# Optimization experiments

Measured on AMD Instinct MI355X. Metric: run time of the kernel, lower is better.

The kernel has to match this reference:

```python
import jax, jax.numpy as jnp
import numpy as np

B, L, D, H = 2, 2048, 1024, 16
HD = D // H
SCALE = HD ** -0.5


def setup_inputs() -> dict:
    key = jax.random.key(0)
    ks = jax.random.split(key, 11)
    s = D ** -0.5  # torch Linear default init scale (uniform bound)
    return {
        "q": jax.random.normal(ks[0], (B, L, D), jnp.float32),
        "k": jax.random.normal(ks[1], (B, L, D), jnp.float32),
        "v": jax.random.normal(ks[2], (B, L, D), jnp.float32),
        "Wq": jax.random.uniform(ks[3], (D, D), jnp.float32, -s, s),
        "bq": jax.random.uniform(ks[4], (D,), jnp.float32, -s, s),
        "Wk": jax.random.uniform(ks[5], (D, D), jnp.float32, -s, s),
        "bk": jax.random.uniform(ks[6], (D,), jnp.float32, -s, s),
        "Wv": jax.random.uniform(ks[7], (D, D), jnp.float32, -s, s),
        "bv": jax.random.uniform(ks[8], (D,), jnp.float32, -s, s),
        "Wo": jax.random.uniform(ks[9], (D, D), jnp.float32, -s, s),
        "bo": jax.random.uniform(ks[10], (D,), jnp.float32, -s, s),
    }


def reference(q, k, v, Wq, bq, Wk, bk, Wv, bv, Wo, bo):
    b, q_len, _ = q.shape
    # projections; weights stored as (D, D) acting on the right: x @ W + b
    qh = (q @ Wq + bq).reshape(b, q_len, H, HD).transpose(0, 2, 1, 3)  # (B,H,Q,hd)
    kh = (k @ Wk + bk).reshape(b, -1, H, HD).transpose(0, 2, 1, 3)    # (B,H,K,hd)
    vh = (v @ Wv + bv).reshape(b, -1, H, HD).transpose(0, 2, 1, 3)    # (B,H,K,hd)
    att = jnp.einsum("bhqd,bhkd->bhqk", qh * SCALE, kh)               # (B,H,Q,K)
    att = jax.nn.softmax(att, axis=-1)
    out = jnp.einsum("bhqk,bhkd->bhqd", att, vh)                      # (B,H,Q,hd)
    out = out.transpose(0, 2, 1, 3).reshape(b, q_len, D)
    return out @ Wo + bo
```

## Files before the change

### kernel.cpp

```cpp
#include <hip/hip_runtime.h>

namespace {
constexpr int kB  = 2;
constexpr int kL  = 2048;
constexpr int kD  = 1024;
constexpr int kH  = 16;
constexpr int kHD = 64;
constexpr int kM  = kB * kL;
}

typedef _Float16 f16x8 __attribute__((ext_vector_type(8)));
typedef float    f32x16 __attribute__((ext_vector_type(16)));
typedef unsigned int u32;

union Frag16 { uint4 u4; unsigned u[4]; f16x8 v; };

__device__ __forceinline__ unsigned short f2h(float f) {
    return __builtin_bit_cast(unsigned short, (_Float16)f);
}
__device__ __forceinline__ unsigned pk2(float a, float b) {
    return __builtin_bit_cast(unsigned, __builtin_amdgcn_cvt_pkrtz(a, b));
}
__device__ __forceinline__ float max3f(float a, float b, float c) {
    float d;
    asm("v_max3_f32 %0, %1, %2, %3" : "=v"(d) : "v"(a), "v"(b), "v"(c));
    return d;
}

__device__ __forceinline__ void gload16(const void* g, void* l) {
    __builtin_amdgcn_global_load_lds(
        (const __attribute__((address_space(1))) u32*)g,
        (__attribute__((address_space(3))) u32*)(unsigned long long)(__builtin_bit_cast(unsigned long long, l)),
        16, 0, 0);
}

__global__ __launch_bounds__(256) void cast_f16_kernel(
    const float* __restrict__ q, const float* __restrict__ k,
    const float* __restrict__ v, unsigned short* __restrict__ dst)
{
    const float* src = blockIdx.y == 0 ? q : (blockIdx.y == 1 ? k : v);
    unsigned short* d = dst + (size_t)blockIdx.y * ((size_t)kM * kD);
    const size_t i = ((size_t)blockIdx.x * 256 + threadIdx.x) * 8;
    const float4 f0 = *(const float4*)(src + i);
    const float4 f1 = *(const float4*)(src + i + 4);
    _Float16 h[8];
    h[0] = (_Float16)f0.x; h[1] = (_Float16)f0.y;
    h[2] = (_Float16)f0.z; h[3] = (_Float16)f0.w;
    h[4] = (_Float16)f1.x; h[5] = (_Float16)f1.y;
    h[6] = (_Float16)f1.z; h[7] = (_Float16)f1.w;
    *(uint4*)(d + i) = *(uint4*)h;
}

__global__ __launch_bounds__(256) void tcast_kernel(
    const float* __restrict__ W0, const float* __restrict__ W1,
    const float* __restrict__ W2, const float* __restrict__ W3,
    unsigned short* __restrict__ WtBase)
{
    __shared__ _Float16 T[64][68];
    const float* W = blockIdx.z == 0 ? W0 : blockIdx.z == 1 ? W1
                   : blockIdx.z == 2 ? W2 : W3;
    unsigned short* Wt = WtBase + (size_t)blockIdx.z * ((size_t)kD * kD);
    const int k0 = blockIdx.y * 64, n0 = blockIdx.x * 64;
    const int tx = threadIdx.x & 15, ty = threadIdx.x >> 4;
#pragma unroll
    for (int i = 0; i < 4; ++i) {
        const int kk = i * 16 + ty;
        const float4 w = *(const float4*)&W[(size_t)(k0 + kk) * kD + n0 + tx * 4];
        T[tx * 4 + 0][kk] = (_Float16)w.x;
        T[tx * 4 + 1][kk] = (_Float16)w.y;
        T[tx * 4 + 2][kk] = (_Float16)w.z;
        T[tx * 4 + 3][kk] = (_Float16)w.w;
    }
    __syncthreads();
#pragma unroll
    for (int i = 0; i < 4; ++i) {
        const int nn = i * 16 + ty;
        *(ushort4*)&Wt[(size_t)(n0 + nn) * kD + k0 + tx * 4] = *(ushort4*)&T[nn][tx * 4];
    }
}

template <int MODE>
__global__ __launch_bounds__(256) void gemm16_kernel(
    const unsigned short* __restrict__ A, const unsigned short* __restrict__ Wt,
    const float* __restrict__ bias, void* __restrict__ Cv)
{
    __shared__ unsigned short Als[3][128 * 32];
    __shared__ unsigned short Bls[3][128 * 32];

    const int tid = threadIdx.x;
    const int lane = tid & 63;
    const int wid = tid >> 6;
    const int l31 = lane & 31;
    const int hi = lane >> 5;
    const int by = blockIdx.x & 31;
    const int bx = blockIdx.x >> 5;
    const int row0 = by * 128;
    const int col0 = bx * 128;
    const int wr = wid >> 1, wc = wid & 1;

    const int srow = wid * 16 + (lane >> 2);
    const int ssl  = lane & 3;
    const int ssrc = (ssl ^ ((srow >> 1) & 3)) * 8;

    const unsigned short* Abase = A + (size_t)(row0 + srow) * kD + ssrc;
    const unsigned short* Bbase = Wt + (size_t)(col0 + srow) * kD + ssrc;

    f32x16 acc00{}, acc01{}, acc10{}, acc11{};

    auto stage = [&](int kt, int buf) {
        gload16(Abase + kt * 32,                   &Als[buf][(wid * 16) * 32]);
        gload16(Abase + (size_t)64 * kD + kt * 32, &Als[buf][(wid * 16 + 64) * 32]);
        gload16(Bbase + kt * 32,                   &Bls[buf][(wid * 16) * 32]);
        gload16(Bbase + (size_t)64 * kD + kt * 32, &Bls[buf][(wid * 16 + 64) * 32]);
    };

    const int ra0 = wr * 64 + l31;
    const int cb0 = wc * 64 + l31;

    stage(0, 0);
    stage(1, 1);
    int cur = 0, stg = 2;
    for (int kt = 0; kt < 32; ++kt) {
        if (kt < 31) asm volatile("s_waitcnt vmcnt(4)" ::: "memory");
        else         asm volatile("s_waitcnt vmcnt(0)" ::: "memory");
        __builtin_amdgcn_s_barrier();
        if (kt + 2 < 32) {
            stage(kt + 2, stg);
            stg = (stg + 1 == 3) ? 0 : stg + 1;
        }
#pragma unroll
        for (int ks = 0; ks < 2; ++ks) {
            const int slot = (ks << 1) | hi;
            Frag16 a0, a1, b0, b1;
            a0.u4 = *(const uint4*)&Als[cur][ra0 * 32 + ((slot ^ ((ra0 >> 1) & 3)) << 3)];
            a1.u4 = *(const uint4*)&Als[cur][(ra0 + 32) * 32 + ((slot ^ (((ra0 + 32) >> 1) & 3)) << 3)];
            b0.u4 = *(const uint4*)&Bls[cur][cb0 * 32 + ((slot ^ ((cb0 >> 1) & 3)) << 3)];
            b1.u4 = *(const uint4*)&Bls[cur][(cb0 + 32) * 32 + ((slot ^ (((cb0 + 32) >> 1) & 3)) << 3)];
            acc00 = __builtin_amdgcn_mfma_f32_32x32x16_f16(a0.v, b0.v, acc00, 0, 0, 0);
            acc01 = __builtin_amdgcn_mfma_f32_32x32x16_f16(a0.v, b1.v, acc01, 0, 0, 0);
            acc10 = __builtin_amdgcn_mfma_f32_32x32x16_f16(a1.v, b0.v, acc10, 0, 0, 0);
            acc11 = __builtin_amdgcn_mfma_f32_32x32x16_f16(a1.v, b1.v, acc11, 0, 0, 0);
        }
        cur = (cur + 1 == 3) ? 0 : cur + 1;
    }

    const float bias0 = bias[col0 + wc * 64 + l31];
    const float bias1 = bias[col0 + wc * 64 + 32 + l31];

    const f32x16* accs[2][2] = {{&acc00, &acc01}, {&acc10, &acc11}};
#pragma unroll
    for (int rt = 0; rt < 2; ++rt) {
#pragma unroll
        for (int ct = 0; ct < 2; ++ct) {
            const f32x16& acv = *accs[rt][ct];
            const float bb = ct ? bias1 : bias0;
            const int c = col0 + wc * 64 + ct * 32 + l31;
            if (MODE == 2) {
                unsigned short* C = (unsigned short*)Cv;
#pragma unroll
                for (int qd = 0; qd < 4; ++qd) {
                    const int r = row0 + wr * 64 + rt * 32 + 8 * qd + 4 * hi;
                    const int b_ = r >> 11, l_ = r & (kL - 1);
                    ushort4 w;
                    w.x = f2h(acv[4 * qd + 0] + bb);
                    w.y = f2h(acv[4 * qd + 1] + bb);
                    w.z = f2h(acv[4 * qd + 2] + bb);
                    w.w = f2h(acv[4 * qd + 3] + bb);
                    *(ushort4*)&C[((size_t)(b_ * kH + (c >> 6)) * kHD + (c & 63)) * kL + l_] = w;
                }
            } else {
#pragma unroll
                for (int reg = 0; reg < 16; ++reg) {
                    const int r = row0 + wr * 64 + rt * 32 + (reg & 3) + 8 * (reg >> 2) + 4 * hi;
                    const float val = acv[reg] + bb;
                    if (MODE == 0) {
                        ((float*)Cv)[(size_t)r * kD + c] = val;
                    } else {
                        const int b_ = r >> 11, l_ = r & (kL - 1);
                        ((unsigned short*)Cv)[((size_t)(b_ * kH + (c >> 6)) * kL + l_) * kHD + (c & 63)] = f2h(val);
                    }
                }
            }
        }
    }
}

__global__ __launch_bounds__(512) void attn_mfma_kernel(
    const unsigned short* __restrict__ Qh, const unsigned short* __restrict__ Kh,
    const unsigned short* __restrict__ Vt, unsigned short* __restrict__ Opart,
    float2* __restrict__ Stat)
{
    __shared__ unsigned short Kls[4][64 * 64];
    __shared__ unsigned short Vls[4][64 * 64];

    const int lane = threadIdx.x & 63;
    const int wid  = threadIdx.x >> 6;
    const int l31  = lane & 31;
    const int hi   = lane >> 5;

    const int id = blockIdx.x;
    const int j  = id >> 3;
    const int bh = (id & 7) * 4 + (j >> 4);
    const int qt = j & 7;
    const int ks = (j >> 3) & 1;
    const int q = qt * 256 + wid * 32 + l31;

    const size_t qkBase = (size_t)bh * kL * kHD;
    const unsigned short* Qp = Qh + qkBase + (size_t)q * kHD + hi * 8;
    Frag16 qf[4];
#pragma unroll
    for (int d = 0; d < 4; ++d) qf[d].u4 = *(const uint4*)(Qp + d * 16);

    const int srow = wid * 8 + (lane >> 3);
    const int soff = (((lane & 7) ^ (srow & 7)) << 3);
    const unsigned short* Kg = Kh + qkBase + (size_t)srow * kHD + soff;
    const unsigned short* Vg = Vt + (size_t)bh * kHD * kL + (size_t)srow * kL + soff;

    auto stage = [&](int kt, int buf) {
        gload16(Kg + (size_t)(kt * 64) * kHD, &Kls[buf][(wid * 8) * 64]);
        gload16(Vg + kt * 64,                 &Vls[buf][(wid * 8) * 64]);
    };

    auto buildpf = [&](const unsigned* u, Frag16* pf) {
        unsigned t0 = hi ? u[0] : u[2];
        unsigned t1 = hi ? u[1] : u[3];
        unsigned t2 = hi ? u[4] : u[6];
        unsigned t3 = hi ? u[5] : u[7];
        const unsigned r0 = __shfl_xor(t0, 32);
        const unsigned r1 = __shfl_xor(t1, 32);
        const unsigned r2 = __shfl_xor(t2, 32);
        const unsigned r3 = __shfl_xor(t3, 32);
        pf[0].u[0] = hi ? r0 : u[0];
        pf[0].u[1] = hi ? r1 : u[1];
        pf[0].u[2] = hi ? u[2] : r0;
        pf[0].u[3] = hi ? u[3] : r1;
        pf[1].u[0] = hi ? r2 : u[4];
        pf[1].u[1] = hi ? r3 : u[5];
        pf[1].u[2] = hi ? u[6] : r2;
        pf[1].u[3] = hi ? u[7] : r3;
    };

    f32x16 o0{}, o1{};
    float m = -1e30f, lsum = 0.f;
    const float cexp = 0.125f * 1.44269504089f;
    const int rA = l31, rB = l31 + 32;

    const int kt0 = ks * 16;
    stage(kt0 + 0, 0);
    stage(kt0 + 1, 1);

    for (int rt = 0; rt < 8; ++rt) {
        const int t0 = 2 * rt;
        asm volatile("s_waitcnt vmcnt(0)" ::: "memory");
        __builtin_amdgcn_s_barrier();
        if (t0 + 3 < 16) {
            stage(kt0 + t0 + 2, (t0 + 2) & 3);
            stage(kt0 + t0 + 3, (t0 + 3) & 3);
        }
        const int bA = t0 & 3, bB = (t0 + 1) & 3;

        f32x16 c0{}, c1{}, c2{}, c3{};
        __builtin_amdgcn_s_setprio(1);
#pragma unroll
        for (int d = 0; d < 4; ++d) {
            const int s = (d << 1) | hi;
            Frag16 ka0, ka1, kb0, kb1;
            ka0.u4 = *(const uint4*)&Kls[bA][rA * 64 + ((s ^ (rA & 7)) << 3)];
            ka1.u4 = *(const uint4*)&Kls[bA][rB * 64 + ((s ^ (rB & 7)) << 3)];
            kb0.u4 = *(const uint4*)&Kls[bB][rA * 64 + ((s ^ (rA & 7)) << 3)];
            kb1.u4 = *(const uint4*)&Kls[bB][rB * 64 + ((s ^ (rB & 7)) << 3)];
            c0 = __builtin_amdgcn_mfma_f32_32x32x16_f16(ka0.v, qf[d].v, c0, 0, 0, 0);
            c1 = __builtin_amdgcn_mfma_f32_32x32x16_f16(ka1.v, qf[d].v, c1, 0, 0, 0);
            c2 = __builtin_amdgcn_mfma_f32_32x32x16_f16(kb0.v, qf[d].v, c2, 0, 0, 0);
            c3 = __builtin_amdgcn_mfma_f32_32x32x16_f16(kb1.v, qf[d].v, c3, 0, 0, 0);
        }
        __builtin_amdgcn_s_setprio(0);

        float mx = fmaxf(fmaxf(c0[0], c1[0]), fmaxf(c2[0], c3[0]));
#pragma unroll
        for (int r = 1; r < 16; ++r) {
            mx = max3f(mx, c0[r], c1[r]);
            mx = max3f(mx, c2[r], c3[r]);
        }
        mx = fmaxf(mx, __shfl_xor(mx, 32));
        if (mx > m + 48.f) {
            const float corr = __builtin_amdgcn_exp2f((m - mx) * cexp);
            m = mx;
            lsum *= corr;
            o0 *= corr;
            o1 *= corr;
        }
        const float mc = m * cexp;

        float rs = 0.f;
        unsigned uA0[8], uA1[8], uB0[8], uB1[8];
#pragma unroll
        for (int i = 0; i < 8; ++i) {
            const float e0 = __builtin_amdgcn_exp2f(fmaf(c0[2 * i], cexp, -mc));
            const float e1 = __builtin_amdgcn_exp2f(fmaf(c0[2 * i + 1], cexp, -mc));
            const float e2 = __builtin_amdgcn_exp2f(fmaf(c1[2 * i], cexp, -mc));
            const float e3 = __builtin_amdgcn_exp2f(fmaf(c1[2 * i + 1], cexp, -mc));
            const float e4 = __builtin_amdgcn_exp2f(fmaf(c2[2 * i], cexp, -mc));
            const float e5 = __builtin_amdgcn_exp2f(fmaf(c2[2 * i + 1], cexp, -mc));
            const float e6 = __builtin_amdgcn_exp2f(fmaf(c3[2 * i], cexp, -mc));
            const float e7 = __builtin_amdgcn_exp2f(fmaf(c3[2 * i + 1], cexp, -mc));
            uA0[i] = pk2(e0, e1);
            uA1[i] = pk2(e2, e3);
            uB0[i] = pk2(e4, e5);
            uB1[i] = pk2(e6, e7);
            rs += ((e0 + e1) + (e2 + e3)) + ((e4 + e5) + (e6 + e7));
        }
        rs += __shfl_xor(rs, 32);
        lsum += rs;

        {
            Frag16 pf[4];
            buildpf(uA0, &pf[0]);
            buildpf(uA1, &pf[2]);
            __builtin_amdgcn_s_setprio(1);
#pragma unroll
            for (int ksl = 0; ksl < 4; ++ksl) {
                const int s = (ksl << 1) | hi;
                Frag16 v0, v1;
                v0.u4 = *(const uint4*)&Vls[bA][rA * 64 + ((s ^ (rA & 7)) << 3)];
                v1.u4 = *(const uint4*)&Vls[bA][rB * 64 + ((s ^ (rB & 7)) << 3)];
                o0 = __builtin_amdgcn_mfma_f32_32x32x16_f16(v0.v, pf[ksl].v, o0, 0, 0, 0);
                o1 = __builtin_amdgcn_mfma_f32_32x32x16_f16(v1.v, pf[ksl].v, o1, 0, 0, 0);
            }
            __builtin_amdgcn_s_setprio(0);
        }
        {
            Frag16 pf[4];
            buildpf(uB0, &pf[0]);
            buildpf(uB1, &pf[2]);
            __builtin_amdgcn_s_setprio(1);
#pragma unroll
            for (int ksl = 0; ksl < 4; ++ksl) {
                const int s = (ksl << 1) | hi;
                Frag16 v0, v1;
                v0.u4 = *(const uint4*)&Vls[bB][rA * 64 + ((s ^ (rA & 7)) << 3)];
                v1.u4 = *(const uint4*)&Vls[bB][rB * 64 + ((s ^ (rB & 7)) << 3)];
                o0 = __builtin_amdgcn_mfma_f32_32x32x16_f16(v0.v, pf[ksl].v, o0, 0, 0, 0);
                o1 = __builtin_amdgcn_mfma_f32_32x32x16_f16(v1.v, pf[ksl].v, o1, 0, 0, 0);
            }
            __builtin_amdgcn_s_setprio(0);
        }
    }

    const size_t prow = (size_t)ks * (32 * kL) + (size_t)bh * kL + q;
    const float inv = 1.f / lsum;
    unsigned short* pp = Opart + prow * kHD;
#pragma unroll
    for (int g = 0; g < 4; ++g) {
        const int d = g * 8 + hi * 4;
        uint2 w0, w1;
        w0.x = pk2(o0[4 * g + 0] * inv, o0[4 * g + 1] * inv);
        w0.y = pk2(o0[4 * g + 2] * inv, o0[4 * g + 3] * inv);
        w1.x = pk2(o1[4 * g + 0] * inv, o1[4 * g + 1] * inv);
        w1.y = pk2(o1[4 * g + 2] * inv, o1[4 * g + 3] * inv);
        *(uint2*)(pp + d) = w0;
        *(uint2*)(pp + 32 + d) = w1;
    }
    if (hi == 0) Stat[prow] = make_float2(m, lsum);
}

__global__ __launch_bounds__(256) void merge_kernel(
    const unsigned short* __restrict__ Opart, const float2* __restrict__ Stat,
    unsigned short* __restrict__ O16)
{
    const int g = blockIdx.x * 256 + threadIdx.x;
    const int row = g >> 3;
    const int d0 = (g & 7) * 8;
    const int bh = row >> 11, q = row & (kL - 1);
    const float2 sa = Stat[row];
    const float2 sb = Stat[32 * kL + row];
    const float cexp = 0.125f * 1.44269504089f;
    const float M = fmaxf(sa.x, sb.x);
    float wa = __builtin_amdgcn_exp2f((sa.x - M) * cexp) * sa.y;
    float wb = __builtin_amdgcn_exp2f((sb.x - M) * cexp) * sb.y;
    const float inv = 1.f / (wa + wb);
    wa *= inv; wb *= inv;

    const unsigned short* pa = Opart + (size_t)row * kHD + d0;
    const unsigned short* pb = pa + (size_t)32 * kL * kHD;
    uint4 ua = *(const uint4*)pa;
    uint4 ub = *(const uint4*)pb;
    _Float16 ha[8], hb[8];
    *(uint4*)ha = ua;
    *(uint4*)hb = ub;
    unsigned out[4];
#pragma unroll
    for (int i = 0; i < 4; ++i) {
        const float v0 = wa * (float)ha[2 * i]     + wb * (float)hb[2 * i];
        const float v1 = wa * (float)ha[2 * i + 1] + wb * (float)hb[2 * i + 1];
        out[i] = pk2(v0, v1);
    }
    const int b_ = bh >> 4, h_ = bh & 15;
    *(uint4*)&O16[((size_t)(b_ * kL + q)) * kD + h_ * kHD + d0] = *(uint4*)out;
}

extern "C" void kernel_launch(void* const* d_in, const int* in_sizes, int n_in,
                              void* d_out, int out_size, void* d_ws, size_t ws_size,
                              hipStream_t stream)
{
    const float* q  = (const float*)d_in[0];
    const float* k  = (const float*)d_in[1];
    const float* v  = (const float*)d_in[2];
    const float* Wq = (const float*)d_in[3];
    const float* bq = (const float*)d_in[4];
    const float* Wk = (const float*)d_in[5];
    const float* bk = (const float*)d_in[6];
    const float* Wv = (const float*)d_in[7];
    const float* bv = (const float*)d_in[8];
    const float* Wo = (const float*)d_in[9];
    const float* bo = (const float*)d_in[10];
    float* out = (float*)d_out;

    const size_t MD = (size_t)kM * kD;
    const size_t DD = (size_t)kD * kD;
    unsigned short* A16 = (unsigned short*)d_ws;
    unsigned short* Wt16 = A16 + 3 * MD;
    unsigned short* Qh16 = Wt16 + 4 * DD;
    unsigned short* Kh16 = Qh16 + MD;
    unsigned short* Vt16 = Kh16 + MD;
    unsigned short* O16   = A16;
    unsigned short* Opart = A16 + MD;
    float2*         Stat  = (float2*)Wt16;

    const dim3 blk(256);

    hipLaunchKernelGGL(cast_f16_kernel, dim3(kM * kD / (256 * 8), 3), blk, 0, stream,
                       q, k, v, A16);
    hipLaunchKernelGGL(tcast_kernel, dim3(16, 16, 4), blk, 0, stream,
                       Wq, Wk, Wv, Wo, Wt16);

    hipLaunchKernelGGL((gemm16_kernel<1>), dim3(256), blk, 0, stream,
                       A16, Wt16, bq, (void*)Qh16);
    hipLaunchKernelGGL((gemm16_kernel<1>), dim3(256), blk, 0, stream,
                       A16 + MD, Wt16 + DD, bk, (void*)Kh16);
    hipLaunchKernelGGL((gemm16_kernel<2>), dim3(256), blk, 0, stream,
                       A16 + 2 * MD, Wt16 + 2 * DD, bv, (void*)Vt16);

    hipLaunchKernelGGL(attn_mfma_kernel, dim3(512), dim3(512), 0, stream,
                       Qh16, Kh16, Vt16, Opart, Stat);
    hipLaunchKernelGGL(merge_kernel, dim3(2048), blk, 0, stream,
                       Opart, Stat, O16);

    hipLaunchKernelGGL((gemm16_kernel<0>), dim3(256), blk, 0, stream,
                       O16, Wt16 + 3 * DD, bo, (void*)out);
}
```

Before: 139.8 us.

## Fuse QKV projection GEMMs into one launch with 128x64 tiles and BK=64

Replaces the three separate QKV GEMM launches with a single kernel that picks the projection from the block index. The tile shape also changes for every GEMM, from 128x128 with BK=32 and a triple buffer to 128x64 with BK=64 and a double buffer. That gives 1536 blocks for QKV and 512 for the output projection, up from 256 each, to fill the CUs better and cut launch overhead. The cost is less reuse per block, since smaller N tiles mean more reads of A, plus a simpler pipeline that waits with __syncthreads instead of explicit vmcnt.

```diff
diff --git a/kernel.cpp b/kernel.cpp
--- a/kernel.cpp
+++ b/kernel.cpp
@@ -79,13 +79,103 @@
     }
 }
 
-template <int MODE>
-__global__ __launch_bounds__(256) void gemm16_kernel(
+__global__ __launch_bounds__(256) void gemm_qkv_kernel(
     const unsigned short* __restrict__ A, const unsigned short* __restrict__ Wt,
-    const float* __restrict__ bias, void* __restrict__ Cv)
-{
-    __shared__ unsigned short Als[3][128 * 32];
-    __shared__ unsigned short Bls[3][128 * 32];
+    const float* __restrict__ bq, const float* __restrict__ bk,
+    const float* __restrict__ bv, unsigned short* __restrict__ Qh,
+    unsigned short* __restrict__ Kh, unsigned short* __restrict__ Vt)
+{
+    __shared__ unsigned short Als[2][128 * 64];
+    __shared__ unsigned short Bls[2][64 * 64];
+
+    const int tid = threadIdx.x;
+    const int lane = tid & 63;
+    const int wid = tid >> 6;
+    const int l31 = lane & 31;
+    const int hi = lane >> 5;
+    const int by = blockIdx.x & 31;
+    const int bxg = blockIdx.x >> 5;
+    const int proj = bxg >> 4;
+    const int row0 = by * 128;
+    const int wr = wid >> 1, wc = wid & 1;
+
+    const int rl = lane >> 3;
+    const int sl = lane & 7;
+    const int ssrc = (sl ^ rl) * 8;
+
+    const unsigned short* Aproj = A + (size_t)proj * ((size_t)kM * kD);
+    const unsigned short* Abase = Aproj + (size_t)(row0 + wid * 32 + rl) * kD + ssrc;
+    const unsigned short* Bbase = Wt + (size_t)(bxg * 64 + wid * 16 + rl) * kD + ssrc;
+
+    f32x16 acc0{}, acc1{};
+
+    auto stage = [&](int kt, int buf) {
+#pragma unroll
+        for (int i = 0; i < 4; ++i)
+            gload16(Abase + (size_t)(i * 8) * kD + kt * 64,
+                    &Als[buf][(wid * 32 + i * 8) * 64]);
+        gload16(Bbase + kt * 64,                   &Bls[buf][(wid * 16) * 64]);
+        gload16(Bbase + (size_t)8 * kD + kt * 64,  &Bls[buf][(wid * 16 + 8) * 64]);
+    };
+
+    const int ra0 = wr * 64 + l31;
+    const int cb0 = wc * 32 + l31;
+
+    stage(0, 0);
+    int cur = 0;
+    for (int kt = 0; kt < kD / 64; ++kt) {
+        __syncthreads();
+        if (kt + 1 < kD / 64) stage(kt + 1, cur ^ 1);
+#pragma unroll
+        for (int ks = 0; ks < 4; ++ks) {
+            const int slot = (ks << 1) | hi;
+            Frag16 a0, a1, b0;
+            a0.u4 = *(const uint4*)&Als[cur][ra0 * 64 + ((slot ^ (ra0 & 7)) << 3)];
+            a1.u4 = *(const uint4*)&Als[cur][(ra0 + 32) * 64 + ((slot ^ ((ra0 + 32) & 7)) << 3)];
+            b0.u4 = *(const uint4*)&Bls[cur][cb0 * 64 + ((slot ^ (cb0 & 7)) << 3)];
+            acc0 = __builtin_amdgcn_mfma_f32_32x32x16_f16(a0.v, b0.v, acc0, 0, 0, 0);
+            acc1 = __builtin_amdgcn_mfma_f32_32x32x16_f16(a1.v, b0.v, acc1, 0, 0, 0);
+        }
+        cur ^= 1;
+    }
+
+    const int n = ((bxg & 15) << 6) + wc * 32 + l31;
+    const float* bias = proj == 0 ? bq : (proj == 1 ? bk : bv);
+    const float bb = bias[n];
+    const f32x16* accs[2] = {&acc0, &acc1};
+#pragma unroll
+    for (int rt = 0; rt < 2; ++rt) {
+        const f32x16& acv = *accs[rt];
+        if (proj == 2) {
+#pragma unroll
+            for (int qd = 0; qd < 4; ++qd) {
+                const int r = row0 + wr * 64 + rt * 32 + 8 * qd + 4 * hi;
+                const int b_ = r >> 11, l_ = r & (kL - 1);
+                ushort4 w;
+                w.x = f2h(acv[4 * qd + 0] + bb);
+                w.y = f2h(acv[4 * qd + 1] + bb);
+                w.z = f2h(acv[4 * qd + 2] + bb);
+                w.w = f2h(acv[4 * qd + 3] + bb);
+                *(ushort4*)&Vt[((size_t)(b_ * kH + (n >> 6)) * kHD + (n & 63)) * kL + l_] = w;
+            }
+        } else {
+            unsigned short* C = proj == 0 ? Qh : Kh;
+#pragma unroll
+            for (int reg = 0; reg < 16; ++reg) {
+                const int r = row0 + wr * 64 + rt * 32 + (reg & 3) + 8 * (reg >> 2) + 4 * hi;
+                const int b_ = r >> 11, l_ = r & (kL - 1);
+                C[((size_t)(b_ * kH + (n >> 6)) * kL + l_) * kHD + (n & 63)] = f2h(acv[reg] + bb);
+            }
+        }
+    }
+}
+
+__global__ __launch_bounds__(256) void gemm_o_kernel(
+    const unsigned short* __restrict__ A, const unsigned short* __restrict__ Wt,
+    const float* __restrict__ bias, float* __restrict__ C)
+{
+    __shared__ unsigned short Als[2][128 * 64];
+    __shared__ unsigned short Bls[2][64 * 64];
 
     const int tid = threadIdx.x;
     const int lane = tid & 63;
@@ -95,92 +185,57 @@
     const int by = blockIdx.x & 31;
     const int bx = blockIdx.x >> 5;
     const int row0 = by * 128;
-    const int col0 = bx * 128;
     const int wr = wid >> 1, wc = wid & 1;
 
-    const int srow = wid * 16 + (lane >> 2);
-    const int ssl  = lane & 3;
-    const int ssrc = (ssl ^ ((srow >> 1) & 3)) * 8;
-
-    const unsigned short* Abase = A + (size_t)(row0 + srow) * kD + ssrc;
-    const unsigned short* Bbase = Wt + (size_t)(col0 + srow) * kD + ssrc;
-
-    f32x16 acc00{}, acc01{}, acc10{}, acc11{};
+    const int rl = lane >> 3;
+    const int sl = lane & 7;
+    const int ssrc = (sl ^ rl) * 8;
+
+    const unsigned short* Abase = A + (size_t)(row0 + wid * 32 + rl) * kD + ssrc;
+    const unsigned short* Bbase = Wt + (size_t)(bx * 64 + wid * 16 + rl) * kD + ssrc;
+
+    f32x16 acc0{}, acc1{};
 
     auto stage = [&](int kt, int buf) {
-        gload16(Abase + kt * 32,                   &Als[buf][(wid * 16) * 32]);
-        gload16(Abase + (size_t)64 * kD + kt * 32, &Als[buf][(wid * 16 + 64) * 32]);
-        gload16(Bbase + kt * 32,                   &Bls[buf][(wid * 16) * 32]);
-        gload16(Bbase + (size_t)64 * kD + kt * 32, &Bls[buf][(wid * 16 + 64) * 32]);
+#pragma unroll
+        for (int i = 0; i < 4; ++i)
+            gload16(Abase + (size_t)(i * 8) * kD + kt * 64,
+                    &Als[buf][(wid * 32 + i * 8) * 64]);
+        gload16(Bbase + kt * 64,                   &Bls[buf][(wid * 16) * 64]);
+        gload16(Bbase + (size_t)8 * kD + kt * 64,  &Bls[buf][(wid * 16 + 8) * 64]);
     };
 
     const int ra0 = wr * 64 + l31;
-    const int cb0 = wc * 64 + l31;
+    const int cb0 = wc * 32 + l31;
 
     stage(0, 0);
-    stage(1, 1);
-    int cur = 0, stg = 2;
-    for (int kt = 0; kt < 32; ++kt) {
-        if (kt < 31) asm volatile("s_waitcnt vmcnt(4)" ::: "memory");
-        else         asm volatile("s_waitcnt vmcnt(0)" ::: "memory");
-        __builtin_amdgcn_s_barrier();
-        if (kt + 2 < 32) {
-            stage(kt + 2, stg);
-            stg = (stg + 1 == 3) ? 0 : stg + 1;
-        }
-#pragma unroll
-        for (int ks = 0; ks < 2; ++ks) {
+    int cur = 0;
+    for (int kt = 0; kt < kD / 64; ++kt) {
+        __syncthreads();
+        if (kt + 1 < kD / 64) stage(kt + 1, cur ^ 1);
+#pragma unroll
+        for (int ks = 0; ks < 4; ++ks) {
             const int slot = (ks << 1) | hi;
-            Frag16 a0, a1, b0, b1;
-            a0.u4 = *(const uint4*)&Als[cur][ra0 * 32 + ((slot ^ ((ra0 >> 1) & 3)) << 3)];
-            a1.u4 = *(const uint4*)&Als[cur][(ra0 + 32) * 32 + ((slot ^ (((ra0 + 32) >> 1) & 3)) << 3)];
-            b0.u4 = *(const uint4*)&Bls[cur][cb0 * 32 + ((slot ^ ((cb0 >> 1) & 3)) << 3)];
-            b1.u4 = *(const uint4*)&Bls[cur][(cb0 + 32) * 32 + ((slot ^ (((cb0 + 32) >> 1) & 3)) << 3)];
-            acc00 = __builtin_amdgcn_mfma_f32_32x32x16_f16(a0.v, b0.v, acc00, 0, 0, 0);
-            acc01 = __builtin_amdgcn_mfma_f32_32x32x16_f16(a0.v, b1.v, acc01, 0, 0, 0);
-            acc10 = __builtin_amdgcn_mfma_f32_32x32x16_f16(a1.v, b0.v, acc10, 0, 0, 0);
-            acc11 = __builtin_amdgcn_mfma_f32_32x32x16_f16(a1.v, b1.v, acc11, 0, 0, 0);
-        }
-        cur = (cur + 1 == 3) ? 0 : cur + 1;
-    }
-
-    const float bias0 = bias[col0 + wc * 64 + l31];
-    const float bias1 = bias[col0 + wc * 64 + 32 + l31];
-
-    const f32x16* accs[2][2] = {{&acc00, &acc01}, {&acc10, &acc11}};
+            Frag16 a0, a1, b0;
+            a0.u4 = *(const uint4*)&Als[cur][ra0 * 64 + ((slot ^ (ra0 & 7)) << 3)];
+            a1.u4 = *(const uint4*)&Als[cur][(ra0 + 32) * 64 + ((slot ^ ((ra0 + 32) & 7)) << 3)];
+            b0.u4 = *(const uint4*)&Bls[cur][cb0 * 64 + ((slot ^ (cb0 & 7)) << 3)];
+            acc0 = __builtin_amdgcn_mfma_f32_32x32x16_f16(a0.v, b0.v, acc0, 0, 0, 0);
+            acc1 = __builtin_amdgcn_mfma_f32_32x32x16_f16(a1.v, b0.v, acc1, 0, 0, 0);
+        }
+        cur ^= 1;
+    }
+
+    const int c = (bx << 6) + wc * 32 + l31;
+    const float bb = bias[c];
+    const f32x16* accs[2] = {&acc0, &acc1};
 #pragma unroll
     for (int rt = 0; rt < 2; ++rt) {
-#pragma unroll
-        for (int ct = 0; ct < 2; ++ct) {
-            const f32x16& acv = *accs[rt][ct];
-            const float bb = ct ? bias1 : bias0;
-            const int c = col0 + wc * 64 + ct * 32 + l31;
-            if (MODE == 2) {
-                unsigned short* C = (unsigned short*)Cv;
-#pragma unroll
-                for (int qd = 0; qd < 4; ++qd) {
-                    const int r = row0 + wr * 64 + rt * 32 + 8 * qd + 4 * hi;
-                    const int b_ = r >> 11, l_ = r & (kL - 1);
-                    ushort4 w;
-                    w.x = f2h(acv[4 * qd + 0] + bb);
-                    w.y = f2h(acv[4 * qd + 1] + bb);
-                    w.z = f2h(acv[4 * qd + 2] + bb);
-                    w.w = f2h(acv[4 * qd + 3] + bb);
-                    *(ushort4*)&C[((size_t)(b_ * kH + (c >> 6)) * kHD + (c & 63)) * kL + l_] = w;
-                }
-            } else {
-#pragma unroll
-                for (int reg = 0; reg < 16; ++reg) {
-                    const int r = row0 + wr * 64 + rt * 32 + (reg & 3) + 8 * (reg >> 2) + 4 * hi;
-                    const float val = acv[reg] + bb;
-                    if (MODE == 0) {
-                        ((float*)Cv)[(size_t)r * kD + c] = val;
-                    } else {
-                        const int b_ = r >> 11, l_ = r & (kL - 1);
-                        ((unsigned short*)Cv)[((size_t)(b_ * kH + (c >> 6)) * kL + l_) * kHD + (c & 63)] = f2h(val);
-                    }
-                }
-            }
+        const f32x16& acv = *accs[rt];
+#pragma unroll
+        for (int reg = 0; reg < 16; ++reg) {
+            const int r = row0 + wr * 64 + rt * 32 + (reg & 3) + 8 * (reg >> 2) + 4 * hi;
+            C[(size_t)r * kD + c] = acv[reg] + bb;
         }
     }
 }
@@ -434,18 +489,14 @@
     hipLaunchKernelGGL(tcast_kernel, dim3(16, 16, 4), blk, 0, stream,
                        Wq, Wk, Wv, Wo, Wt16);
 
-    hipLaunchKernelGGL((gemm16_kernel<1>), dim3(256), blk, 0, stream,
-                       A16, Wt16, bq, (void*)Qh16);
-    hipLaunchKernelGGL((gemm16_kernel<1>), dim3(256), blk, 0, stream,
-                       A16 + MD, Wt16 + DD, bk, (void*)Kh16);
-    hipLaunchKernelGGL((gemm16_kernel<2>), dim3(256), blk, 0, stream,
-                       A16 + 2 * MD, Wt16 + 2 * DD, bv, (void*)Vt16);
+    hipLaunchKernelGGL(gemm_qkv_kernel, dim3(32 * 48), blk, 0, stream,
+                       A16, Wt16, bq, bk, bv, Qh16, Kh16, Vt16);
 
     hipLaunchKernelGGL(attn_mfma_kernel, dim3(512), dim3(512), 0, stream,
                        Qh16, Kh16, Vt16, Opart, Stat);
     hipLaunchKernelGGL(merge_kernel, dim3(2048), blk, 0, stream,
                        Opart, Stat, O16);
 
-    hipLaunchKernelGGL((gemm16_kernel<0>), dim3(256), blk, 0, stream,
-                       O16, Wt16 + 3 * DD, bo, (void*)out);
-}
+    hipLaunchKernelGGL(gemm_o_kernel, dim3(32 * 16), blk, 0, stream,
+                       O16, Wt16 + 3 * DD, bo, out);
+}
```

After: 136.5 us. -2.4%, faster.
